# Optimization experiments

Measured on AMD Instinct MI355X. Metric: run time of the kernel, lower is better.

The kernel has to match this reference:

```python
import jax, jax.numpy as jnp
import numpy as np

HIDDEN = 64
N_LAYERS = 3
WORLD_W = 1.0
WORLD_H = 1.0

silu = jax.nn.silu


def _lin(x, w, b):
    return x @ w + b


def setup_inputs() -> dict:
    key = jax.random.key(0)
    ks = jax.random.split(key, 32)
    B, N, H, L = 2, 512, HIDDEN, N_LAYERS
    s = 0.05
    inp = {
        "state": jax.random.uniform(ks[0], (B, N, 4), dtype=jnp.float32),
        "h_init_w": jax.random.normal(ks[1], (1, H), dtype=jnp.float32) * s,
        "h_init_b": jnp.zeros((H,), jnp.float32),
        # per-layer stacked params (L, ...)
        "edge_w1": jax.random.normal(ks[2], (L, 2 * H + 4, H), jnp.float32) * s,
        "edge_b1": jnp.zeros((L, H), jnp.float32),
        "edge_w2": jax.random.normal(ks[3], (L, H, H), jnp.float32) * s,
        "edge_b2": jnp.zeros((L, H), jnp.float32),
        "force_w1": jax.random.normal(ks[4], (L, H, H), jnp.float32) * s,
        "force_b1": jnp.zeros((L, H), jnp.float32),
        "force_w2": jax.random.normal(ks[5], (L, H, 1), jnp.float32) * s,
        "force_b2": jnp.zeros((L, 1), jnp.float32),
        "node_w1": jax.random.normal(ks[6], (L, 2 * H, H), jnp.float32) * s,
        "node_b1": jnp.zeros((L, H), jnp.float32),
        "node_w2": jax.random.normal(ks[7], (L, H, H), jnp.float32) * s,
        "node_b2": jnp.zeros((L, H), jnp.float32),
        "wall_w1": jax.random.normal(ks[8], (H + 4, H), jnp.float32) * s,
        "wall_b1": jnp.zeros((H,), jnp.float32),
        "wall_w2": jax.random.normal(ks[9], (H, H), jnp.float32) * s,
        "wall_b2": jnp.zeros((H,), jnp.float32),
        "wall_w3": jax.random.normal(ks[10], (H, 4), jnp.float32) * s,
        "wall_b3": jnp.zeros((4,), jnp.float32),
    }
    return inp


def _layer(h, pos, vel, ew1, eb1, ew2, eb2, fw1, fb1, fw2, fb2, nw1, nb1, nw2, nb2):
    B, N, H = h.shape
    # rel_pos[b,i,j] = pos[b,j] - pos[b,i]
    rel_pos = pos[:, None, :, :] - pos[:, :, None, :]          # (B,N,N,2)
    dist_sq = jnp.sum(rel_pos ** 2, axis=-1, keepdims=True)    # (B,N,N,1)
    dist = jnp.sqrt(dist_sq + 1e-8)
    normal = rel_pos / dist
    speed_sq = jnp.sum(vel ** 2, axis=-1, keepdims=True)       # (B,N,1)
    rel_vel = vel[:, None, :, :] - vel[:, :, None, :]
    approach = jnp.sum(rel_vel * normal, axis=-1, keepdims=True)
    h_i = jnp.broadcast_to(h[:, :, None, :], (B, N, N, H))
    h_j = jnp.broadcast_to(h[:, None, :, :], (B, N, N, H))
    sp_i = jnp.broadcast_to(speed_sq[:, :, None, :], (B, N, N, 1))
    sp_j = jnp.broadcast_to(speed_sq[:, None, :, :], (B, N, N, 1))
    edge_feat = jnp.concatenate([h_i, h_j, dist_sq, sp_i, sp_j, approach], axis=-1)
    m_ij = silu(_lin(silu(_lin(edge_feat, ew1, eb1)), ew2, eb2))  # (B,N,N,H)
    force_weight = _lin(silu(_lin(m_ij, fw1, fb1)), fw2, fb2)     # (B,N,N,1)
    mask = (1.0 - jnp.eye(N, dtype=h.dtype))[None, :, :, None]
    force = jnp.sum(force_weight * normal * mask, axis=2)         # (B,N,2)
    m_agg = jnp.sum(m_ij * mask, axis=2)                          # (B,N,H)
    h_new = _lin(silu(_lin(jnp.concatenate([h, m_agg], axis=-1), nw1, nb1)), nw2, nb2)
    return h_new, force


def reference(state, h_init_w, h_init_b, edge_w1, edge_b1, edge_w2, edge_b2,
              force_w1, force_b1, force_w2, force_b2,
              node_w1, node_b1, node_w2, node_b2,
              wall_w1, wall_b1, wall_w2, wall_b2, wall_w3, wall_b3):
    pos = state[:, :, :2]
    vel = state[:, :, 2:]
    speed = jnp.sqrt(jnp.sum(vel ** 2, axis=-1, keepdims=True))
    h = silu(_lin(speed, h_init_w, h_init_b))
    total_force = jnp.zeros_like(pos)
    for l in range(edge_w1.shape[0]):
        h, f = _layer(h, pos, vel,
                      edge_w1[l], edge_b1[l], edge_w2[l], edge_b2[l],
                      force_w1[l], force_b1[l], force_w2[l], force_b2[l],
                      node_w1[l], node_b1[l], node_w2[l], node_b2[l])
        total_force = total_force + f
    wall_dists = jnp.stack([pos[:, :, 0], WORLD_W - pos[:, :, 0],
                            pos[:, :, 1], WORLD_H - pos[:, :, 1]], axis=-1)
    x = jnp.concatenate([h, wall_dists], axis=-1)
    wall_mag = _lin(silu(_lin(silu(_lin(x, wall_w1, wall_b1)), wall_w2, wall_b2)), wall_w3, wall_b3)  # (B,N,4)
    wall_normals = jnp.array([[1.0, 0.0], [-1.0, 0.0], [0.0, 1.0], [0.0, -1.0]], dtype=state.dtype)
    wall_force = jnp.einsum('bnw,wd->bnd', wall_mag, wall_normals)
    return total_force + wall_force
```

## Files before the change

### kernel.cpp

```cpp
#include <hip/hip_runtime.h>
#include <math.h>

#define H 64
#define NN 512
#define NB 2
#define NL 3
#define NBLK (NN * NB)

typedef _Float16 half8  __attribute__((ext_vector_type(8)));
typedef __fp16   fp16x2 __attribute__((ext_vector_type(2)));
typedef float    float4v __attribute__((ext_vector_type(4)));

union FragU { half8 h; unsigned int u[4]; uint4 q4; };
union F8    { float4 v4[2]; float f[8]; };

__device__ __forceinline__ float silu_f(float x) {
    float e = __expf(-x);
    return x * __builtin_amdgcn_rcpf(1.0f + e);
}

__device__ __forceinline__ unsigned int pk2(float a, float b) {
    fp16x2 h = __builtin_amdgcn_cvt_pkrtz(a, b);
    return __builtin_bit_cast(unsigned int, h);
}

__global__ __launch_bounds__(256) void k_setup(
    const float* __restrict__ state, const float* __restrict__ hiw,
    const float* __restrict__ hib, const float* __restrict__ ew1,
    const float* __restrict__ eb1, const float* __restrict__ ew2,
    const float* __restrict__ fw1, float* __restrict__ h,
    float* __restrict__ P, float* __restrict__ Q, float* __restrict__ faccum,
    uint4* __restrict__ wpack)
{
    const int bn  = blockIdx.x;
    const int tid = threadIdx.x;
    const int wv  = tid >> 6;
    const int lane = tid & 63;

    __shared__ float sh[64];
    __shared__ float sRed[4][64];
    __shared__ float sRedQ[4][64];

    if (tid < 64) {
        const float* st = state + bn * 4;
        float vx = st[2], vy = st[3];
        float s2 = vx * vx + vy * vy;
        if (tid < 2) faccum[bn * 2 + tid] = 0.0f;
        float hv = silu_f(sqrtf(s2) * hiw[tid] + hib[tid]);
        h[(size_t)bn * H + tid] = hv;
        sh[tid] = hv;
    }
    if (bn < 6) {
        const int pl = bn >> 1, mat = bn & 1;
        const float* src = (mat ? fw1 : ew2) + (size_t)pl * 4096;
        uint4* dst = wpack + ((size_t)pl * 2 + mat) * 512;
        for (int g = tid; g < 512; g += 256) {
            int f = g >> 6, ln = g & 63;
            int mt = f >> 1, kt = f & 1, qq = ln >> 4, mm = ln & 15;
            int cm  = mt * 16 + mm;
            int cin = kt * 32 + qq * 8;
            uint4 u;
            u.x = pk2(src[(cin + 0) * 64 + cm], src[(cin + 1) * 64 + cm]);
            u.y = pk2(src[(cin + 2) * 64 + cm], src[(cin + 3) * 64 + cm]);
            u.z = pk2(src[(cin + 4) * 64 + cm], src[(cin + 5) * 64 + cm]);
            u.w = pk2(src[(cin + 6) * 64 + cm], src[(cin + 7) * 64 + cm]);
            dst[g] = u;
        }
    }
    __syncthreads();

    {
        float pp = 0.0f, qp = 0.0f;
        const float* wp = ew1 + (size_t)(wv * 16) * 64 + lane;
        const float* wq = ew1 + (size_t)(64 + wv * 16) * 64 + lane;
#pragma unroll 8
        for (int k = 0; k < 16; k++) {
            float hk = sh[wv * 16 + k];
            pp += hk * wp[(size_t)k * 64];
            qp += hk * wq[(size_t)k * 64];
        }
        sRed[wv][lane]  = pp;
        sRedQ[wv][lane] = qp;
    }
    __syncthreads();
    if (wv == 0) {
        const float* st = state + bn * 4;
        float vx = st[2], vy = st[3];
        float s2 = vx * vx + vy * vy;
        P[(size_t)bn * 64 + lane] = eb1[lane] + sRed[0][lane] + sRed[1][lane]
                                  + sRed[2][lane] + sRed[3][lane];
        Q[(size_t)bn * 64 + lane] = sRedQ[0][lane] + sRedQ[1][lane]
                                  + sRedQ[2][lane] + sRedQ[3][lane]
                                  + s2 * ew1[130 * 64 + lane];
    }
}

__global__ __launch_bounds__(256) void k_edge(
    const float* __restrict__ state,
    const float* __restrict__ P, const float* __restrict__ Q,
    float* __restrict__ Pout, float* __restrict__ Qout,
    const float* __restrict__ ew1_l,
    const uint4* __restrict__ wpackL,
    const float* __restrict__ eb2_l,
    const float* __restrict__ fb1_l,
    const float* __restrict__ fw2_l, const float* __restrict__ fb2_l,
    float* __restrict__ h, float* __restrict__ faccum,
    const float* __restrict__ nw1_l, const float* __restrict__ nb1_l,
    const float* __restrict__ nw2_l, const float* __restrict__ nb2_l,
    const float* __restrict__ ew1_n, const float* __restrict__ eb1_n,
    const float* __restrict__ ww1, const float* __restrict__ wb1,
    const float* __restrict__ ww2, const float* __restrict__ wb2,
    const float* __restrict__ ww3, const float* __restrict__ wb3,
    float* __restrict__ out, int last)
{
    const int i    = blockIdx.x;
    const int b    = blockIdx.y;
    const int tid  = threadIdx.x;
    const int wv   = tid >> 6;
    const int lane = tid & 63;
    const int q    = lane >> 4;
    const int m    = lane & 15;
    const int bn_i = b * NN + i;

    __shared__ float sW[128];
    __shared__ float sBias[192];
    __shared__ float sPB[64];
    __shared__ unsigned short sMT[4][16 * 72];
    __shared__ float sRed[4][64];
    __shared__ float sRedQ[4][64];
    __shared__ float sF[4][2];

    if (tid < 128) sW[tid] = ew1_l[(128 + (tid >> 6) * 3) * 64 + (tid & 63)];
    if (tid < 192) sBias[tid] = (tid < 64) ? eb2_l[tid]
                              : (tid < 128) ? fb1_l[tid - 64]
                              : fw2_l[tid - 128];

    FragU wreg[8], freg[8];
#pragma unroll
    for (int f = 0; f < 8; f++) {
        wreg[f].q4 = wpackL[f * 64 + lane];
        freg[f].q4 = wpackL[512 + f * 64 + lane];
    }

    const float4 sti = *(const float4*)&state[(size_t)bn_i * 4];
    const float  spi = sti.z * sti.z + sti.w * sti.w;
    if (tid < 64) sPB[tid] = P[(size_t)bn_i * 64 + tid] + spi * ew1_l[129 * 64 + tid];
    __syncthreads();

    const float fb2q = fb2_l[0] * 0.25f;

    float maccp[16];
#pragma unroll
    for (int t = 0; t < 16; t++) maccp[t] = 0.0f;
    float fax = 0.0f, fay = 0.0f;

    unsigned short* MT = sMT[wv];

#pragma unroll 1
    for (int ck = 0; ck < 8; ck++) {
        unsigned swoff = 0;
        asm volatile("" : "+v"(swoff));
        __builtin_assume((swoff & 3u) == 0);

        const int jg = wv * 128 + ck * 16 + m;

        float jnx, jny;
        FragU xb[2];
        {
            const float4 stj = *(const float4*)&state[(size_t)(b * NN + jg) * 4];
            float dx = stj.x - sti.x, dy = stj.y - sti.y;
            float ds = dx * dx + dy * dy;
            float rs = __builtin_amdgcn_rsqf(ds + 1e-8f);
            jnx = dx * rs;
            jny = dy * rs;
            float jap = (stj.z - sti.z) * jnx + (stj.w - sti.w) * jny;

#pragma unroll
            for (int kt = 0; kt < 2; kt++) {
                const int c0 = kt * 32 + q * 8;
                F8 w0, w3, pb;
                w0.v4[0] = *(const float4*)&sW[swoff + c0];
                w0.v4[1] = *(const float4*)&sW[swoff + c0 + 4];
                w3.v4[0] = *(const float4*)&sW[swoff + 64 + c0];
                w3.v4[1] = *(const float4*)&sW[swoff + 64 + c0 + 4];
                pb.v4[0] = *(const float4*)&sPB[swoff + c0];
                pb.v4[1] = *(const float4*)&sPB[swoff + c0 + 4];

                const float* Qr = &Q[(size_t)(b * NN + jg) * 64 + c0];
                F8 qv;
                qv.v4[0] = *(const float4*)Qr;
                qv.v4[1] = *(const float4*)(Qr + 4);
                float xv[8];
#pragma unroll
                for (int d = 0; d < 8; d++) {
                    float pre = pb.f[d] + qv.f[d] + ds * w0.f[d]
                              + jap * w3.f[d];
                    xv[d] = silu_f(pre);
                }
#pragma unroll
                for (int d = 0; d < 4; d++)
                    xb[kt].u[d] = pk2(xv[2 * d], xv[2 * d + 1]);
            }
        }

#pragma unroll
        for (int hf = 0; hf < 2; hf++) {
            float4v acc[2];
#pragma unroll
            for (int mt2 = 0; mt2 < 2; mt2++) {
                const float4 b2v = *(const float4*)&sBias[swoff + (hf * 2 + mt2) * 16 + q * 4];
                acc[mt2][0] = b2v.x; acc[mt2][1] = b2v.y;
                acc[mt2][2] = b2v.z; acc[mt2][3] = b2v.w;
            }
#pragma unroll
            for (int kt = 0; kt < 2; kt++) {
#pragma unroll
                for (int mt2 = 0; mt2 < 2; mt2++) {
                    acc[mt2] = __builtin_amdgcn_mfma_f32_16x16x32_f16(
                        wreg[(hf * 2 + mt2) * 2 + kt].h, xb[kt].h, acc[mt2], 0, 0, 0);
                }
            }
#pragma unroll
            for (int mt2 = 0; mt2 < 2; mt2++) {
                const int mt = hf * 2 + mt2;
                float4v a = acc[mt2];
                float m0 = silu_f(a[0]);
                float m1 = silu_f(a[1]);
                float m2 = silu_f(a[2]);
                float m3 = silu_f(a[3]);
                if (jg != i) {
                    maccp[mt * 4 + 0] += m0;
                    maccp[mt * 4 + 1] += m1;
                    maccp[mt * 4 + 2] += m2;
                    maccp[mt * 4 + 3] += m3;
                }
                uint2 dw = make_uint2(pk2(m0, m1), pk2(m2, m3));
                *(uint2*)&MT[m * 72 + mt * 16 + q * 4] = dw;
            }
        }

        float fdp = 0.0f;
        FragU xb2[2];
#pragma unroll
        for (int kt = 0; kt < 2; kt++)
            xb2[kt].q4 = *(uint4*)&MT[m * 72 + kt * 32 + q * 8];
#pragma unroll
        for (int hf = 0; hf < 2; hf++) {
            float4v acc2[2];
#pragma unroll
            for (int mt2 = 0; mt2 < 2; mt2++) {
                const float4 fb1v = *(const float4*)&sBias[swoff + 64 + (hf * 2 + mt2) * 16 + q * 4];
                acc2[mt2][0] = fb1v.x; acc2[mt2][1] = fb1v.y;
                acc2[mt2][2] = fb1v.z; acc2[mt2][3] = fb1v.w;
            }
#pragma unroll
            for (int kt = 0; kt < 2; kt++) {
#pragma unroll
                for (int mt2 = 0; mt2 < 2; mt2++) {
                    acc2[mt2] = __builtin_amdgcn_mfma_f32_16x16x32_f16(
                        freg[(hf * 2 + mt2) * 2 + kt].h, xb2[kt].h, acc2[mt2], 0, 0, 0);
                }
            }
#pragma unroll
            for (int mt2 = 0; mt2 < 2; mt2++) {
                const float4 fw2v = *(const float4*)&sBias[swoff + 128 + (hf * 2 + mt2) * 16 + q * 4];
                float4v a = acc2[mt2];
                fdp += silu_f(a[0]) * fw2v.x
                     + silu_f(a[1]) * fw2v.y
                     + silu_f(a[2]) * fw2v.z
                     + silu_f(a[3]) * fw2v.w;
            }
        }

        {
            float fd = fdp + fb2q;
            fax += fd * jnx;
            fay += fd * jny;
        }
    }

#pragma unroll
    for (int t = 0; t < 16; t++) {
        float v = maccp[t];
        v += __shfl_xor(v, 1, 64);
        v += __shfl_xor(v, 2, 64);
        v += __shfl_xor(v, 4, 64);
        v += __shfl_xor(v, 8, 64);
        maccp[t] = v;
    }
    if (m == 0) {
#pragma unroll
        for (int mt = 0; mt < 4; mt++)
#pragma unroll
          for (int r = 0; r < 4; r++)
            sRed[wv][mt * 16 + q * 4 + r] = maccp[mt * 4 + r];
    }
#pragma unroll
    for (int off = 1; off < 64; off <<= 1) {
        fax += __shfl_xor(fax, off, 64);
        fay += __shfl_xor(fay, off, 64);
    }
    if (lane == 0) {
        sF[wv][0] = fax;
        sF[wv][1] = fay;
    }
    __syncthreads();

    float* scr = (float*)sMT;
    const int c = lane;
    if (wv == 0) {
        float magg = sRed[0][c] + sRed[1][c] + sRed[2][c] + sRed[3][c];
        scr[c]      = h[(size_t)bn_i * 64 + c];
        scr[64 + c] = magg;
    }
    __syncthreads();

    {
        float part = 0.0f;
        const float* w = nw1_l + (size_t)(wv * 32) * 64 + c;
#pragma unroll 8
        for (int k = 0; k < 32; k++) part += scr[wv * 32 + k] * w[(size_t)k * 64];
        sRed[wv][c] = part;
    }
    __syncthreads();
    if (wv == 0) {
        float t1 = nb1_l[c] + sRed[0][c] + sRed[1][c] + sRed[2][c] + sRed[3][c];
        scr[128 + c] = silu_f(t1);
    }
    __syncthreads();

    {
        float part = 0.0f;
        const float* w = nw2_l + (size_t)(wv * 16) * 64 + c;
#pragma unroll 8
        for (int k = 0; k < 16; k++) part += scr[128 + wv * 16 + k] * w[(size_t)k * 64];
        sRed[wv][c] = part;
    }
    __syncthreads();

    if (wv == 0) {
        float hn  = nb2_l[c] + sRed[0][c] + sRed[1][c] + sRed[2][c] + sRed[3][c];
        scr[192 + c] = hn;
        if (!last) {
            h[(size_t)bn_i * 64 + c] = hn;
            float fxl = sF[0][0] + sF[1][0] + sF[2][0] + sF[3][0];
            float fyl = sF[0][1] + sF[1][1] + sF[2][1] + sF[3][1];
            if (c == 0) {
                faccum[bn_i * 2 + 0] += fxl;
                faccum[bn_i * 2 + 1] += fyl;
            }
        }
    }
    __syncthreads();

    if (!last) {
        float pp = 0.0f, qp = 0.0f;
        const float* wp = ew1_n + (size_t)(wv * 16) * 64 + c;
        const float* wq = ew1_n + (size_t)(64 + wv * 16) * 64 + c;
#pragma unroll 8
        for (int k = 0; k < 16; k++) {
            float hk = scr[192 + wv * 16 + k];
            pp += hk * wp[(size_t)k * 64];
            qp += hk * wq[(size_t)k * 64];
        }
        sRed[wv][c]  = pp;
        sRedQ[wv][c] = qp;
        __syncthreads();
        if (wv == 0) {
            Pout[(size_t)bn_i * 64 + c] = eb1_n[c] + sRed[0][c] + sRed[1][c]
                                        + sRed[2][c] + sRed[3][c];
            Qout[(size_t)bn_i * 64 + c] = sRedQ[0][c] + sRedQ[1][c]
                                        + sRedQ[2][c] + sRedQ[3][c]
                                        + spi * ew1_n[130 * 64 + c];
        }
        return;
    }

    if (wv != 0) return;

    if (c < 4) {
        float px = sti.x, py = sti.y;
        float wd = (c == 0) ? px : (c == 1) ? 1.0f - px : (c == 2) ? py : 1.0f - py;
        scr[256 + c] = wd;
    }
    float t2 = wb1[c];
#pragma unroll 4
    for (int k = 0; k < 64; k++) t2 += scr[192 + k] * ww1[k * 64 + c];
#pragma unroll
    for (int k = 0; k < 4; k++)  t2 += scr[256 + k] * ww1[(64 + k) * 64 + c];
    t2 = silu_f(t2);
    scr[320 + c] = t2;
    float u = wb2[c];
#pragma unroll 8
    for (int k = 0; k < 64; k++) u += scr[320 + k] * ww2[k * 64 + c];
    u = silu_f(u);
    scr[384 + c] = u;
    if (c < 4) {
        float mg = wb3[c];
        for (int k = 0; k < 64; k++) mg += scr[384 + k] * ww3[k * 4 + c];
        scr[448 + c] = mg;
    }
    if (c == 0) {
        float fxl = sF[0][0] + sF[1][0] + sF[2][0] + sF[3][0];
        float fyl = sF[0][1] + sF[1][1] + sF[2][1] + sF[3][1];
        float fx = faccum[bn_i * 2 + 0] + fxl + (scr[448 + 0] - scr[448 + 1]);
        float fy = faccum[bn_i * 2 + 1] + fyl + (scr[448 + 2] - scr[448 + 3]);
        out[bn_i * 2 + 0] = fx;
        out[bn_i * 2 + 1] = fy;
    }
}

extern "C" void kernel_launch(void* const* d_in, const int* in_sizes, int n_in,
                              void* d_out, int out_size, void* d_ws, size_t ws_size,
                              hipStream_t stream)
{
    const float* state = (const float*)d_in[0];
    const float* hiw   = (const float*)d_in[1];
    const float* hib   = (const float*)d_in[2];
    const float* ew1   = (const float*)d_in[3];
    const float* eb1   = (const float*)d_in[4];
    const float* ew2   = (const float*)d_in[5];
    const float* eb2   = (const float*)d_in[6];
    const float* fw1   = (const float*)d_in[7];
    const float* fb1   = (const float*)d_in[8];
    const float* fw2   = (const float*)d_in[9];
    const float* fb2   = (const float*)d_in[10];
    const float* nw1   = (const float*)d_in[11];
    const float* nb1   = (const float*)d_in[12];
    const float* nw2   = (const float*)d_in[13];
    const float* nb2   = (const float*)d_in[14];
    const float* ww1   = (const float*)d_in[15];
    const float* wb1   = (const float*)d_in[16];
    const float* ww2   = (const float*)d_in[17];
    const float* wb2   = (const float*)d_in[18];
    const float* ww3   = (const float*)d_in[19];
    const float* wb3   = (const float*)d_in[20];
    float* out = (float*)d_out;

    float* ws     = (float*)d_ws;
    float* h      = ws;
    float* P0     = h      + (size_t)NB * NN * H;
    float* Q0     = P0     + (size_t)NB * NN * H;
    float* P1     = Q0     + (size_t)NB * NN * H;
    float* Q1     = P1     + (size_t)NB * NN * H;
    float* faccum = Q1     + (size_t)NB * NN * H;
    float* wpackf = faccum + (size_t)NB * NN * 2;
    uint4* wpack  = (uint4*)(((uintptr_t)wpackf + 15) & ~(uintptr_t)15);

    float* Pb[2] = { P0, P1 };
    float* Qb[2] = { Q0, Q1 };

    k_setup<<<NBLK, 256, 0, stream>>>(state, hiw, hib, ew1, eb1,
                                      ew2, fw1, h, P0, Q0, faccum, wpack);

    for (int l = 0; l < NL; l++) {
        const int last = (l == NL - 1) ? 1 : 0;
        const int nl = last ? 0 : (l + 1);
        const int cur = l & 1, nxt = (l + 1) & 1;
        k_edge<<<dim3(NN, NB), 256, 0, stream>>>(
            state, Pb[cur], Qb[cur], Pb[nxt], Qb[nxt],
            ew1 + (size_t)l * 132 * 64,
            wpack + (size_t)l * 1024,
            eb2 + (size_t)l * 64,
            fb1 + (size_t)l * 64,
            fw2 + (size_t)l * 64, fb2 + (size_t)l,
            h, faccum,
            nw1 + (size_t)l * 128 * 64, nb1 + (size_t)l * 64,
            nw2 + (size_t)l * 64 * 64,  nb2 + (size_t)l * 64,
            ew1 + (size_t)nl * 132 * 64, eb1 + (size_t)nl * 64,
            ww1, wb1, ww2, wb2, ww3, wb3,
            out, last);
    }
}
```

Measured before the change: 236.8 us.

## Software-pipeline edge MLP chunks with double-buffered LDS tile

Restructures the per-wave chunk loop into a front stage (edge features plus first MFMA layer, writing to LDS) and a back stage (force MLP reading the previous chunk's tile). LDS is double-buffered so the force stage of chunk ck-1 can interleave with the edge stage of chunk ck, hiding the LDS write-to-read latency and the MFMA dependency chains. It also adds a min-blocks-per-CU hint of 4 to launch_bounds. In exchange the kernel uses more LDS and carries fragments across iterations, which raises register pressure and could cause spills under the tighter occupancy bound.

```diff
diff --git a/kernel.cpp b/kernel.cpp
--- a/kernel.cpp
+++ b/kernel.cpp
@@ -95,7 +95,7 @@
     }
 }
 
-__global__ __launch_bounds__(256) void k_edge(
+__global__ __launch_bounds__(256, 4) void k_edge(
     const float* __restrict__ state,
     const float* __restrict__ P, const float* __restrict__ Q,
     float* __restrict__ Pout, float* __restrict__ Qout,
@@ -125,7 +125,7 @@
     __shared__ float sW[128];
     __shared__ float sBias[192];
     __shared__ float sPB[64];
-    __shared__ unsigned short sMT[4][16 * 72];
+    __shared__ __align__(16) unsigned short sMTd[2][4][16 * 72];
     __shared__ float sRed[4][64];
     __shared__ float sRedQ[4][64];
     __shared__ float sF[4][2];
@@ -154,26 +154,25 @@
     for (int t = 0; t < 16; t++) maccp[t] = 0.0f;
     float fax = 0.0f, fay = 0.0f;
 
-    unsigned short* MT = sMT[wv];
-
-#pragma unroll 1
-    for (int ck = 0; ck < 8; ck++) {
+    FragU xb2[2];
+    float pjnx, pjny;
+
+    auto do_front = [&](int ck, float& jnx_o, float& jny_o) {
         unsigned swoff = 0;
         asm volatile("" : "+v"(swoff));
         __builtin_assume((swoff & 3u) == 0);
 
         const int jg = wv * 128 + ck * 16 + m;
 
-        float jnx, jny;
         FragU xb[2];
         {
             const float4 stj = *(const float4*)&state[(size_t)(b * NN + jg) * 4];
             float dx = stj.x - sti.x, dy = stj.y - sti.y;
             float ds = dx * dx + dy * dy;
             float rs = __builtin_amdgcn_rsqf(ds + 1e-8f);
-            jnx = dx * rs;
-            jny = dy * rs;
-            float jap = (stj.z - sti.z) * jnx + (stj.w - sti.w) * jny;
+            jnx_o = dx * rs;
+            jny_o = dy * rs;
+            float jap = (stj.z - sti.z) * jnx_o + (stj.w - sti.w) * jny_o;
 
 #pragma unroll
             for (int kt = 0; kt < 2; kt++) {
@@ -202,6 +201,8 @@
                     xb[kt].u[d] = pk2(xv[2 * d], xv[2 * d + 1]);
             }
         }
+
+        unsigned short* MT = sMTd[ck & 1][wv];
 
 #pragma unroll
         for (int hf = 0; hf < 2; hf++) {
@@ -238,12 +239,14 @@
                 *(uint2*)&MT[m * 72 + mt * 16 + q * 4] = dw;
             }
         }
+    };
+
+    auto do_back = [&](float jnxp, float jnyp) {
+        unsigned swoff = 0;
+        asm volatile("" : "+v"(swoff));
+        __builtin_assume((swoff & 3u) == 0);
 
         float fdp = 0.0f;
-        FragU xb2[2];
-#pragma unroll
-        for (int kt = 0; kt < 2; kt++)
-            xb2[kt].q4 = *(uint4*)&MT[m * 72 + kt * 32 + q * 8];
 #pragma unroll
         for (int hf = 0; hf < 2; hf++) {
             float4v acc2[2];
@@ -271,12 +274,29 @@
                      + silu_f(a[3]) * fw2v.w;
             }
         }
-
+        float fd = fdp + fb2q;
+        fax += fd * jnxp;
+        fay += fd * jnyp;
+    };
+
+    do_front(0, pjnx, pjny);
+#pragma unroll 1
+    for (int ck = 1; ck < 8; ck++) {
         {
-            float fd = fdp + fb2q;
-            fax += fd * jnx;
-            fay += fd * jny;
-        }
+            const unsigned short* MTp = sMTd[(ck + 1) & 1][wv];
+            xb2[0].q4 = *(const uint4*)&MTp[m * 72 + q * 8];
+            xb2[1].q4 = *(const uint4*)&MTp[m * 72 + 32 + q * 8];
+        }
+        float jnx, jny;
+        do_front(ck, jnx, jny);
+        do_back(pjnx, pjny);
+        pjnx = jnx; pjny = jny;
+    }
+    {
+        const unsigned short* MTp = sMTd[1][wv];
+        xb2[0].q4 = *(const uint4*)&MTp[m * 72 + q * 8];
+        xb2[1].q4 = *(const uint4*)&MTp[m * 72 + 32 + q * 8];
+        do_back(pjnx, pjny);
     }
 
 #pragma unroll
@@ -306,7 +326,7 @@
     }
     __syncthreads();
 
-    float* scr = (float*)sMT;
+    float* scr = (float*)sMTd;
     const int c = lane;
     if (wv == 0) {
         float magg = sRed[0][c] + sRed[1][c] + sRed[2][c] + sRed[3][c];
```

After: 289.0 us. 22.0% more time.

## Process two receiver nodes per block with 512 threads to share neighbor loads

Applied to the files above, without the earlier changes.

Each k_edge block now handles two i-nodes with eight waves instead of one node with four waves. Every wave sweeps 64 neighbors and reuses each neighbor's state and Q row for both nodes. The node-update tail is split so that each group of four waves serves one node. The aim is to halve per-block setup work (weight fragment loads, bias staging) and the global Q traffic per pair. In exchange, registers and LDS per block roughly double, which may lower occupancy, and the grid shrinks to 512 blocks.

```diff
diff --git a/kernel.cpp b/kernel.cpp
--- a/kernel.cpp
+++ b/kernel.cpp
@@ -95,7 +95,7 @@
     }
 }
 
-__global__ __launch_bounds__(256) void k_edge(
+__global__ __launch_bounds__(512) void k_edge(
     const float* __restrict__ state,
     const float* __restrict__ P, const float* __restrict__ Q,
     float* __restrict__ Pout, float* __restrict__ Qout,
@@ -113,22 +113,22 @@
     const float* __restrict__ ww3, const float* __restrict__ wb3,
     float* __restrict__ out, int last)
 {
-    const int i    = blockIdx.x;
+    const int ip   = blockIdx.x;
     const int b    = blockIdx.y;
     const int tid  = threadIdx.x;
     const int wv   = tid >> 6;
     const int lane = tid & 63;
     const int q    = lane >> 4;
     const int m    = lane & 15;
-    const int bn_i = b * NN + i;
+    const int bn0  = b * NN + ip * 2;
 
     __shared__ float sW[128];
     __shared__ float sBias[192];
-    __shared__ float sPB[64];
-    __shared__ unsigned short sMT[4][16 * 72];
-    __shared__ float sRed[4][64];
-    __shared__ float sRedQ[4][64];
-    __shared__ float sF[4][2];
+    __shared__ float sPB[2][64];
+    __shared__ __align__(16) unsigned short sMT[8][2][16 * 72];
+    __shared__ float sRed[2][8][64];
+    __shared__ float sRedQ[2][4][64];
+    __shared__ float sF[8][4];
 
     if (tid < 128) sW[tid] = ew1_l[(128 + (tid >> 6) * 3) * 64 + (tid & 63)];
     if (tid < 192) sBias[tid] = (tid < 64) ? eb2_l[tid]
@@ -142,212 +142,255 @@
         freg[f].q4 = wpackL[512 + f * 64 + lane];
     }
 
-    const float4 sti = *(const float4*)&state[(size_t)bn_i * 4];
-    const float  spi = sti.z * sti.z + sti.w * sti.w;
-    if (tid < 64) sPB[tid] = P[(size_t)bn_i * 64 + tid] + spi * ew1_l[129 * 64 + tid];
+    const float4 sti0 = *(const float4*)&state[(size_t)bn0 * 4];
+    const float4 sti1 = *(const float4*)&state[(size_t)(bn0 + 1) * 4];
+    const float  spi0 = sti0.z * sti0.z + sti0.w * sti0.w;
+    const float  spi1 = sti1.z * sti1.z + sti1.w * sti1.w;
+    if (tid < 128) {
+        const int ci = tid >> 6, c = tid & 63;
+        const float sp = ci ? spi1 : spi0;
+        sPB[ci][c] = P[(size_t)(bn0 + ci) * 64 + c] + sp * ew1_l[129 * 64 + c];
+    }
     __syncthreads();
 
     const float fb2q = fb2_l[0] * 0.25f;
 
-    float maccp[16];
-#pragma unroll
-    for (int t = 0; t < 16; t++) maccp[t] = 0.0f;
-    float fax = 0.0f, fay = 0.0f;
-
-    unsigned short* MT = sMT[wv];
+    float maccp[2][16];
+#pragma unroll
+    for (int ii = 0; ii < 2; ii++)
+#pragma unroll
+        for (int t = 0; t < 16; t++) maccp[ii][t] = 0.0f;
+    float fax[2] = {0.0f, 0.0f}, fay[2] = {0.0f, 0.0f};
 
 #pragma unroll 1
-    for (int ck = 0; ck < 8; ck++) {
+    for (int ck = 0; ck < 4; ck++) {
         unsigned swoff = 0;
         asm volatile("" : "+v"(swoff));
         __builtin_assume((swoff & 3u) == 0);
 
-        const int jg = wv * 128 + ck * 16 + m;
-
-        float jnx, jny;
-        FragU xb[2];
+        const int jg = wv * 64 + ck * 16 + m;
+
+        const float4 stj = *(const float4*)&state[(size_t)(b * NN + jg) * 4];
+        float jnx[2], jny[2], dsv[2], jap[2];
         {
-            const float4 stj = *(const float4*)&state[(size_t)(b * NN + jg) * 4];
-            float dx = stj.x - sti.x, dy = stj.y - sti.y;
-            float ds = dx * dx + dy * dy;
-            float rs = __builtin_amdgcn_rsqf(ds + 1e-8f);
-            jnx = dx * rs;
-            jny = dy * rs;
-            float jap = (stj.z - sti.z) * jnx + (stj.w - sti.w) * jny;
-
-#pragma unroll
-            for (int kt = 0; kt < 2; kt++) {
-                const int c0 = kt * 32 + q * 8;
-                F8 w0, w3, pb;
-                w0.v4[0] = *(const float4*)&sW[swoff + c0];
-                w0.v4[1] = *(const float4*)&sW[swoff + c0 + 4];
-                w3.v4[0] = *(const float4*)&sW[swoff + 64 + c0];
-                w3.v4[1] = *(const float4*)&sW[swoff + 64 + c0 + 4];
-                pb.v4[0] = *(const float4*)&sPB[swoff + c0];
-                pb.v4[1] = *(const float4*)&sPB[swoff + c0 + 4];
-
-                const float* Qr = &Q[(size_t)(b * NN + jg) * 64 + c0];
-                F8 qv;
-                qv.v4[0] = *(const float4*)Qr;
-                qv.v4[1] = *(const float4*)(Qr + 4);
-                float xv[8];
-#pragma unroll
-                for (int d = 0; d < 8; d++) {
-                    float pre = pb.f[d] + qv.f[d] + ds * w0.f[d]
-                              + jap * w3.f[d];
-                    xv[d] = silu_f(pre);
-                }
-#pragma unroll
-                for (int d = 0; d < 4; d++)
-                    xb[kt].u[d] = pk2(xv[2 * d], xv[2 * d + 1]);
+            float dx = stj.x - sti0.x, dy = stj.y - sti0.y;
+            float d2 = dx * dx + dy * dy;
+            float rs = __builtin_amdgcn_rsqf(d2 + 1e-8f);
+            jnx[0] = dx * rs; jny[0] = dy * rs; dsv[0] = d2;
+            jap[0] = (stj.z - sti0.z) * jnx[0] + (stj.w - sti0.w) * jny[0];
+        }
+        {
+            float dx = stj.x - sti1.x, dy = stj.y - sti1.y;
+            float d2 = dx * dx + dy * dy;
+            float rs = __builtin_amdgcn_rsqf(d2 + 1e-8f);
+            jnx[1] = dx * rs; jny[1] = dy * rs; dsv[1] = d2;
+            jap[1] = (stj.z - sti1.z) * jnx[1] + (stj.w - sti1.w) * jny[1];
+        }
+
+        FragU xb[2][2];
+#pragma unroll
+        for (int kt = 0; kt < 2; kt++) {
+            const int c0 = kt * 32 + q * 8;
+            F8 w0, w3, pb0, pb1;
+            w0.v4[0] = *(const float4*)&sW[swoff + c0];
+            w0.v4[1] = *(const float4*)&sW[swoff + c0 + 4];
+            w3.v4[0] = *(const float4*)&sW[swoff + 64 + c0];
+            w3.v4[1] = *(const float4*)&sW[swoff + 64 + c0 + 4];
+            pb0.v4[0] = *(const float4*)&sPB[0][swoff + c0];
+            pb0.v4[1] = *(const float4*)&sPB[0][swoff + c0 + 4];
+            pb1.v4[0] = *(const float4*)&sPB[1][swoff + c0];
+            pb1.v4[1] = *(const float4*)&sPB[1][swoff + c0 + 4];
+
+            const float* Qr = &Q[(size_t)(b * NN + jg) * 64 + c0];
+            F8 qv;
+            qv.v4[0] = *(const float4*)Qr;
+            qv.v4[1] = *(const float4*)(Qr + 4);
+
+            float xv0[8], xv1[8];
+#pragma unroll
+            for (int d = 0; d < 8; d++) {
+                float base = qv.f[d];
+                float w0d = w0.f[d], w3d = w3.f[d];
+                float pre0 = pb0.f[d] + base + dsv[0] * w0d + jap[0] * w3d;
+                float pre1 = pb1.f[d] + base + dsv[1] * w0d + jap[1] * w3d;
+                xv0[d] = silu_f(pre0);
+                xv1[d] = silu_f(pre1);
             }
-        }
-
-#pragma unroll
-        for (int hf = 0; hf < 2; hf++) {
-            float4v acc[2];
-#pragma unroll
-            for (int mt2 = 0; mt2 < 2; mt2++) {
-                const float4 b2v = *(const float4*)&sBias[swoff + (hf * 2 + mt2) * 16 + q * 4];
-                acc[mt2][0] = b2v.x; acc[mt2][1] = b2v.y;
-                acc[mt2][2] = b2v.z; acc[mt2][3] = b2v.w;
+#pragma unroll
+            for (int d = 0; d < 4; d++) {
+                xb[0][kt].u[d] = pk2(xv0[2 * d], xv0[2 * d + 1]);
+                xb[1][kt].u[d] = pk2(xv1[2 * d], xv1[2 * d + 1]);
             }
-#pragma unroll
-            for (int kt = 0; kt < 2; kt++) {
+        }
+
+#pragma unroll
+        for (int ii = 0; ii < 2; ii++) {
+            unsigned short* MT = sMT[wv][ii];
+            const int inode = ip * 2 + ii;
+#pragma unroll
+            for (int hf = 0; hf < 2; hf++) {
+                float4v acc[2];
 #pragma unroll
                 for (int mt2 = 0; mt2 < 2; mt2++) {
-                    acc[mt2] = __builtin_amdgcn_mfma_f32_16x16x32_f16(
-                        wreg[(hf * 2 + mt2) * 2 + kt].h, xb[kt].h, acc[mt2], 0, 0, 0);
+                    const float4 b2v = *(const float4*)&sBias[swoff + (hf * 2 + mt2) * 16 + q * 4];
+                    acc[mt2][0] = b2v.x; acc[mt2][1] = b2v.y;
+                    acc[mt2][2] = b2v.z; acc[mt2][3] = b2v.w;
+                }
+#pragma unroll
+                for (int kt = 0; kt < 2; kt++) {
+#pragma unroll
+                    for (int mt2 = 0; mt2 < 2; mt2++) {
+                        acc[mt2] = __builtin_amdgcn_mfma_f32_16x16x32_f16(
+                            wreg[(hf * 2 + mt2) * 2 + kt].h, xb[ii][kt].h, acc[mt2], 0, 0, 0);
+                    }
+                }
+#pragma unroll
+                for (int mt2 = 0; mt2 < 2; mt2++) {
+                    const int mt = hf * 2 + mt2;
+                    float4v a = acc[mt2];
+                    float m0 = silu_f(a[0]);
+                    float m1 = silu_f(a[1]);
+                    float m2 = silu_f(a[2]);
+                    float m3 = silu_f(a[3]);
+                    if (jg != inode) {
+                        maccp[ii][mt * 4 + 0] += m0;
+                        maccp[ii][mt * 4 + 1] += m1;
+                        maccp[ii][mt * 4 + 2] += m2;
+                        maccp[ii][mt * 4 + 3] += m3;
+                    }
+                    uint2 dw = make_uint2(pk2(m0, m1), pk2(m2, m3));
+                    *(uint2*)&MT[m * 72 + mt * 16 + q * 4] = dw;
                 }
             }
-#pragma unroll
-            for (int mt2 = 0; mt2 < 2; mt2++) {
-                const int mt = hf * 2 + mt2;
-                float4v a = acc[mt2];
-                float m0 = silu_f(a[0]);
-                float m1 = silu_f(a[1]);
-                float m2 = silu_f(a[2]);
-                float m3 = silu_f(a[3]);
-                if (jg != i) {
-                    maccp[mt * 4 + 0] += m0;
-                    maccp[mt * 4 + 1] += m1;
-                    maccp[mt * 4 + 2] += m2;
-                    maccp[mt * 4 + 3] += m3;
-                }
-                uint2 dw = make_uint2(pk2(m0, m1), pk2(m2, m3));
-                *(uint2*)&MT[m * 72 + mt * 16 + q * 4] = dw;
+        }
+
+#pragma unroll
+        for (int ii = 0; ii < 2; ii++) {
+            const unsigned short* MT = sMT[wv][ii];
+            FragU xb2[2];
+            xb2[0].q4 = *(const uint4*)&MT[m * 72 + q * 8];
+            xb2[1].q4 = *(const uint4*)&MT[m * 72 + 32 + q * 8];
+            float fdp = 0.0f;
+#pragma unroll
+            for (int hf = 0; hf < 2; hf++) {
+                float4v acc2[2];
+#pragma unroll
+                for (int mt2 = 0; mt2 < 2; mt2++) {
+                    const float4 fb1v = *(const float4*)&sBias[swoff + 64 + (hf * 2 + mt2) * 16 + q * 4];
+                    acc2[mt2][0] = fb1v.x; acc2[mt2][1] = fb1v.y;
+                    acc2[mt2][2] = fb1v.z; acc2[mt2][3] = fb1v.w;
+                }
+#pragma unroll
+                for (int kt = 0; kt < 2; kt++) {
+#pragma unroll
+                    for (int mt2 = 0; mt2 < 2; mt2++) {
+                        acc2[mt2] = __builtin_amdgcn_mfma_f32_16x16x32_f16(
+                            freg[(hf * 2 + mt2) * 2 + kt].h, xb2[kt].h, acc2[mt2], 0, 0, 0);
+                    }
+                }
+#pragma unroll
+                for (int mt2 = 0; mt2 < 2; mt2++) {
+                    const float4 fw2v = *(const float4*)&sBias[swoff + 128 + (hf * 2 + mt2) * 16 + q * 4];
+                    float4v a = acc2[mt2];
+                    fdp += silu_f(a[0]) * fw2v.x
+                         + silu_f(a[1]) * fw2v.y
+                         + silu_f(a[2]) * fw2v.z
+                         + silu_f(a[3]) * fw2v.w;
+                }
             }
-        }
-
-        float fdp = 0.0f;
-        FragU xb2[2];
-#pragma unroll
-        for (int kt = 0; kt < 2; kt++)
-            xb2[kt].q4 = *(uint4*)&MT[m * 72 + kt * 32 + q * 8];
-#pragma unroll
-        for (int hf = 0; hf < 2; hf++) {
-            float4v acc2[2];
-#pragma unroll
-            for (int mt2 = 0; mt2 < 2; mt2++) {
-                const float4 fb1v = *(const float4*)&sBias[swoff + 64 + (hf * 2 + mt2) * 16 + q * 4];
-                acc2[mt2][0] = fb1v.x; acc2[mt2][1] = fb1v.y;
-                acc2[mt2][2] = fb1v.z; acc2[mt2][3] = fb1v.w;
-            }
-#pragma unroll
-            for (int kt = 0; kt < 2; kt++) {
-#pragma unroll
-                for (int mt2 = 0; mt2 < 2; mt2++) {
-                    acc2[mt2] = __builtin_amdgcn_mfma_f32_16x16x32_f16(
-                        freg[(hf * 2 + mt2) * 2 + kt].h, xb2[kt].h, acc2[mt2], 0, 0, 0);
-                }
-            }
-#pragma unroll
-            for (int mt2 = 0; mt2 < 2; mt2++) {
-                const float4 fw2v = *(const float4*)&sBias[swoff + 128 + (hf * 2 + mt2) * 16 + q * 4];
-                float4v a = acc2[mt2];
-                fdp += silu_f(a[0]) * fw2v.x
-                     + silu_f(a[1]) * fw2v.y
-                     + silu_f(a[2]) * fw2v.z
-                     + silu_f(a[3]) * fw2v.w;
-            }
-        }
-
-        {
             float fd = fdp + fb2q;
-            fax += fd * jnx;
-            fay += fd * jny;
-        }
-    }
-
-#pragma unroll
-    for (int t = 0; t < 16; t++) {
-        float v = maccp[t];
-        v += __shfl_xor(v, 1, 64);
-        v += __shfl_xor(v, 2, 64);
-        v += __shfl_xor(v, 4, 64);
-        v += __shfl_xor(v, 8, 64);
-        maccp[t] = v;
-    }
+            fax[ii] += fd * jnx[ii];
+            fay[ii] += fd * jny[ii];
+        }
+    }
+
+#pragma unroll
+    for (int ii = 0; ii < 2; ii++)
+#pragma unroll
+        for (int t = 0; t < 16; t++) {
+            float v = maccp[ii][t];
+            v += __shfl_xor(v, 1, 64);
+            v += __shfl_xor(v, 2, 64);
+            v += __shfl_xor(v, 4, 64);
+            v += __shfl_xor(v, 8, 64);
+            maccp[ii][t] = v;
+        }
     if (m == 0) {
 #pragma unroll
-        for (int mt = 0; mt < 4; mt++)
-#pragma unroll
-          for (int r = 0; r < 4; r++)
-            sRed[wv][mt * 16 + q * 4 + r] = maccp[mt * 4 + r];
+        for (int ii = 0; ii < 2; ii++)
+#pragma unroll
+            for (int mt = 0; mt < 4; mt++)
+#pragma unroll
+                for (int r = 0; r < 4; r++)
+                    sRed[ii][wv][mt * 16 + q * 4 + r] = maccp[ii][mt * 4 + r];
     }
 #pragma unroll
     for (int off = 1; off < 64; off <<= 1) {
-        fax += __shfl_xor(fax, off, 64);
-        fay += __shfl_xor(fay, off, 64);
+        fax[0] += __shfl_xor(fax[0], off, 64);
+        fay[0] += __shfl_xor(fay[0], off, 64);
+        fax[1] += __shfl_xor(fax[1], off, 64);
+        fay[1] += __shfl_xor(fay[1], off, 64);
     }
     if (lane == 0) {
-        sF[wv][0] = fax;
-        sF[wv][1] = fay;
-    }
-    __syncthreads();
-
-    float* scr = (float*)sMT;
+        sF[wv][0] = fax[0]; sF[wv][1] = fay[0];
+        sF[wv][2] = fax[1]; sF[wv][3] = fay[1];
+    }
+    __syncthreads();
+
+    const int ii  = wv >> 2;
+    const int wv4 = wv & 3;
+    const int bnI = bn0 + ii;
+    float* scrI = ((float*)sMT) + ii * 1024;
     const int c = lane;
-    if (wv == 0) {
-        float magg = sRed[0][c] + sRed[1][c] + sRed[2][c] + sRed[3][c];
-        scr[c]      = h[(size_t)bn_i * 64 + c];
-        scr[64 + c] = magg;
+
+    if (wv4 == 0) {
+        float magg = 0.0f;
+#pragma unroll
+        for (int w = 0; w < 8; w++) magg += sRed[ii][w][c];
+        scrI[c]      = h[(size_t)bnI * 64 + c];
+        scrI[64 + c] = magg;
     }
     __syncthreads();
 
     {
         float part = 0.0f;
-        const float* w = nw1_l + (size_t)(wv * 32) * 64 + c;
+        const float* w = nw1_l + (size_t)(wv4 * 32) * 64 + c;
 #pragma unroll 8
-        for (int k = 0; k < 32; k++) part += scr[wv * 32 + k] * w[(size_t)k * 64];
-        sRed[wv][c] = part;
-    }
-    __syncthreads();
-    if (wv == 0) {
-        float t1 = nb1_l[c] + sRed[0][c] + sRed[1][c] + sRed[2][c] + sRed[3][c];
-        scr[128 + c] = silu_f(t1);
+        for (int k = 0; k < 32; k++) part += scrI[wv4 * 32 + k] * w[(size_t)k * 64];
+        sRed[ii][wv4][c] = part;
+    }
+    __syncthreads();
+    if (wv4 == 0) {
+        float t1 = nb1_l[c] + sRed[ii][0][c] + sRed[ii][1][c]
+                 + sRed[ii][2][c] + sRed[ii][3][c];
+        scrI[128 + c] = silu_f(t1);
     }
     __syncthreads();
 
     {
         float part = 0.0f;
-        const float* w = nw2_l + (size_t)(wv * 16) * 64 + c;
+        const float* w = nw2_l + (size_t)(wv4 * 16) * 64 + c;
 #pragma unroll 8
-        for (int k = 0; k < 16; k++) part += scr[128 + wv * 16 + k] * w[(size_t)k * 64];
-        sRed[wv][c] = part;
-    }
-    __syncthreads();
-
-    if (wv == 0) {
-        float hn  = nb2_l[c] + sRed[0][c] + sRed[1][c] + sRed[2][c] + sRed[3][c];
-        scr[192 + c] = hn;
+        for (int k = 0; k < 16; k++) part += scrI[128 + wv4 * 16 + k] * w[(size_t)k * 64];
+        sRed[ii][wv4][c] = part;
+    }
+    __syncthreads();
+
+    if (wv4 == 0) {
+        float hn = nb2_l[c] + sRed[ii][0][c] + sRed[ii][1][c]
+                 + sRed[ii][2][c] + sRed[ii][3][c];
+        scrI[192 + c] = hn;
         if (!last) {
-            h[(size_t)bn_i * 64 + c] = hn;
-            float fxl = sF[0][0] + sF[1][0] + sF[2][0] + sF[3][0];
-            float fyl = sF[0][1] + sF[1][1] + sF[2][1] + sF[3][1];
+            h[(size_t)bnI * 64 + c] = hn;
             if (c == 0) {
-                faccum[bn_i * 2 + 0] += fxl;
-                faccum[bn_i * 2 + 1] += fyl;
+                float fxl = 0.0f, fyl = 0.0f;
+#pragma unroll
+                for (int w = 0; w < 8; w++) {
+                    fxl += sF[w][ii * 2 + 0];
+                    fyl += sF[w][ii * 2 + 1];
+                }
+                faccum[bnI * 2 + 0] += fxl;
+                faccum[bnI * 2 + 1] += fyl;
             }
         }
     }
@@ -355,58 +398,67 @@
 
     if (!last) {
         float pp = 0.0f, qp = 0.0f;
-        const float* wp = ew1_n + (size_t)(wv * 16) * 64 + c;
-        const float* wq = ew1_n + (size_t)(64 + wv * 16) * 64 + c;
+        const float* wp = ew1_n + (size_t)(wv4 * 16) * 64 + c;
+        const float* wq = ew1_n + (size_t)(64 + wv4 * 16) * 64 + c;
 #pragma unroll 8
         for (int k = 0; k < 16; k++) {
-            float hk = scr[192 + wv * 16 + k];
+            float hk = scrI[192 + wv4 * 16 + k];
             pp += hk * wp[(size_t)k * 64];
             qp += hk * wq[(size_t)k * 64];
         }
-        sRed[wv][c]  = pp;
-        sRedQ[wv][c] = qp;
+        sRed[ii][wv4][c]  = pp;
+        sRedQ[ii][wv4][c] = qp;
         __syncthreads();
-        if (wv == 0) {
-            Pout[(size_t)bn_i * 64 + c] = eb1_n[c] + sRed[0][c] + sRed[1][c]
-                                        + sRed[2][c] + sRed[3][c];
-            Qout[(size_t)bn_i * 64 + c] = sRedQ[0][c] + sRedQ[1][c]
-                                        + sRedQ[2][c] + sRedQ[3][c]
-                                        + spi * ew1_n[130 * 64 + c];
+        if (wv4 == 0) {
+            const float spiI = ii ? spi1 : spi0;
+            Pout[(size_t)bnI * 64 + c] = eb1_n[c] + sRed[ii][0][c] + sRed[ii][1][c]
+                                       + sRed[ii][2][c] + sRed[ii][3][c];
+            Qout[(size_t)bnI * 64 + c] = sRedQ[ii][0][c] + sRedQ[ii][1][c]
+                                       + sRedQ[ii][2][c] + sRedQ[ii][3][c]
+                                       + spiI * ew1_n[130 * 64 + c];
         }
         return;
     }
 
-    if (wv != 0) return;
-
-    if (c < 4) {
-        float px = sti.x, py = sti.y;
-        float wd = (c == 0) ? px : (c == 1) ? 1.0f - px : (c == 2) ? py : 1.0f - py;
-        scr[256 + c] = wd;
+    if (wv4 != 0) return;
+
+    {
+        const float pxI = ii ? sti1.x : sti0.x;
+        const float pyI = ii ? sti1.y : sti0.y;
+        if (c < 4) {
+            float wd = (c == 0) ? pxI : (c == 1) ? 1.0f - pxI
+                     : (c == 2) ? pyI : 1.0f - pyI;
+            scrI[256 + c] = wd;
+        }
     }
     float t2 = wb1[c];
 #pragma unroll 4
-    for (int k = 0; k < 64; k++) t2 += scr[192 + k] * ww1[k * 64 + c];
-#pragma unroll
-    for (int k = 0; k < 4; k++)  t2 += scr[256 + k] * ww1[(64 + k) * 64 + c];
+    for (int k = 0; k < 64; k++) t2 += scrI[192 + k] * ww1[k * 64 + c];
+#pragma unroll
+    for (int k = 0; k < 4; k++)  t2 += scrI[256 + k] * ww1[(64 + k) * 64 + c];
     t2 = silu_f(t2);
-    scr[320 + c] = t2;
+    scrI[320 + c] = t2;
     float u = wb2[c];
 #pragma unroll 8
-    for (int k = 0; k < 64; k++) u += scr[320 + k] * ww2[k * 64 + c];
+    for (int k = 0; k < 64; k++) u += scrI[320 + k] * ww2[k * 64 + c];
     u = silu_f(u);
-    scr[384 + c] = u;
+    scrI[384 + c] = u;
     if (c < 4) {
         float mg = wb3[c];
-        for (int k = 0; k < 64; k++) mg += scr[384 + k] * ww3[k * 4 + c];
-        scr[448 + c] = mg;
+        for (int k = 0; k < 64; k++) mg += scrI[384 + k] * ww3[k * 4 + c];
+        scrI[448 + c] = mg;
     }
     if (c == 0) {
-        float fxl = sF[0][0] + sF[1][0] + sF[2][0] + sF[3][0];
-        float fyl = sF[0][1] + sF[1][1] + sF[2][1] + sF[3][1];
-        float fx = faccum[bn_i * 2 + 0] + fxl + (scr[448 + 0] - scr[448 + 1]);
-        float fy = faccum[bn_i * 2 + 1] + fyl + (scr[448 + 2] - scr[448 + 3]);
-        out[bn_i * 2 + 0] = fx;
-        out[bn_i * 2 + 1] = fy;
+        float fxl = 0.0f, fyl = 0.0f;
+#pragma unroll
+        for (int w = 0; w < 8; w++) {
+            fxl += sF[w][ii * 2 + 0];
+            fyl += sF[w][ii * 2 + 1];
+        }
+        float fx = faccum[bnI * 2 + 0] + fxl + (scrI[448 + 0] - scrI[448 + 1]);
+        float fy = faccum[bnI * 2 + 1] + fyl + (scrI[448 + 2] - scrI[448 + 3]);
+        out[bnI * 2 + 0] = fx;
+        out[bnI * 2 + 1] = fy;
     }
 }
 
@@ -457,7 +509,7 @@
         const int last = (l == NL - 1) ? 1 : 0;
         const int nl = last ? 0 : (l + 1);
         const int cur = l & 1, nxt = (l + 1) & 1;
-        k_edge<<<dim3(NN, NB), 256, 0, stream>>>(
+        k_edge<<<dim3(NN / 2, NB), 512, 0, stream>>>(
             state, Pb[cur], Qb[cur], Pb[nxt], Qb[nxt],
             ew1 + (size_t)l * 132 * 64,
             wpack + (size_t)l * 1024,
```

Measured after the change: 243.5 us. 2.8% more time.

## Split each node's edge loop across two blocks with atomic last-block reduction

Applied to the files above, without the earlier changes.

Doubles the edge-kernel grid so each node's 512 neighbours are split between two blocks, each handling 256 j's. Partial message sums and forces are combined through global atomics, and a per-node counter picks the last-finishing block to run the node MLP and produce the next P/Q. The second-stage MFMA weight fragments move from registers into LDS to lower register pressure. The aim is more parallelism and occupancy per layer. The cost is extra global atomics, a threadfence, zero-initialised scratch buffers, and more LDS use.

```diff
diff --git a/kernel.cpp b/kernel.cpp
--- a/kernel.cpp
+++ b/kernel.cpp
@@ -30,7 +30,8 @@
     const float* __restrict__ eb1, const float* __restrict__ ew2,
     const float* __restrict__ fw1, float* __restrict__ h,
     float* __restrict__ P, float* __restrict__ Q, float* __restrict__ faccum,
-    uint4* __restrict__ wpack)
+    uint4* __restrict__ wpack, float* __restrict__ mpart,
+    unsigned* __restrict__ cntb)
 {
     const int bn  = blockIdx.x;
     const int tid = threadIdx.x;
@@ -40,6 +41,9 @@
     __shared__ float sh[64];
     __shared__ float sRed[4][64];
     __shared__ float sRedQ[4][64];
+
+    if (tid < 192) mpart[((size_t)(tid >> 6) * NBLK + bn) * 64 + (tid & 63)] = 0.0f;
+    if (tid >= 192 && tid < 195) cntb[(size_t)(tid - 192) * NBLK + bn] = 0u;
 
     if (tid < 64) {
         const float* st = state + bn * 4;
@@ -105,6 +109,7 @@
     const float* __restrict__ fb1_l,
     const float* __restrict__ fw2_l, const float* __restrict__ fb2_l,
     float* __restrict__ h, float* __restrict__ faccum,
+    float* __restrict__ mpartL, unsigned* __restrict__ cntL,
     const float* __restrict__ nw1_l, const float* __restrict__ nb1_l,
     const float* __restrict__ nw2_l, const float* __restrict__ nb2_l,
     const float* __restrict__ ew1_n, const float* __restrict__ eb1_n,
@@ -114,7 +119,9 @@
     float* __restrict__ out, int last)
 {
     const int i    = blockIdx.x;
-    const int b    = blockIdx.y;
+    const int bh   = blockIdx.y;
+    const int b    = bh >> 1;
+    const int half = bh & 1;
     const int tid  = threadIdx.x;
     const int wv   = tid >> 6;
     const int lane = tid & 63;
@@ -125,22 +132,23 @@
     __shared__ float sW[128];
     __shared__ float sBias[192];
     __shared__ float sPB[64];
-    __shared__ unsigned short sMT[4][16 * 72];
+    __shared__ __align__(16) unsigned short sMT[4][16 * 72];
+    __shared__ uint4 sFreg[512];
     __shared__ float sRed[4][64];
     __shared__ float sRedQ[4][64];
     __shared__ float sF[4][2];
+    __shared__ int   sLast;
 
     if (tid < 128) sW[tid] = ew1_l[(128 + (tid >> 6) * 3) * 64 + (tid & 63)];
     if (tid < 192) sBias[tid] = (tid < 64) ? eb2_l[tid]
                               : (tid < 128) ? fb1_l[tid - 64]
                               : fw2_l[tid - 128];
 
-    FragU wreg[8], freg[8];
-#pragma unroll
-    for (int f = 0; f < 8; f++) {
-        wreg[f].q4 = wpackL[f * 64 + lane];
-        freg[f].q4 = wpackL[512 + f * 64 + lane];
-    }
+    FragU wreg[8];
+#pragma unroll
+    for (int f = 0; f < 8; f++) wreg[f].q4 = wpackL[f * 64 + lane];
+    sFreg[tid]       = wpackL[512 + tid];
+    sFreg[256 + tid] = wpackL[512 + 256 + tid];
 
     const float4 sti = *(const float4*)&state[(size_t)bn_i * 4];
     const float  spi = sti.z * sti.z + sti.w * sti.w;
@@ -154,15 +162,13 @@
     for (int t = 0; t < 16; t++) maccp[t] = 0.0f;
     float fax = 0.0f, fay = 0.0f;
 
-    unsigned short* MT = sMT[wv];
-
 #pragma unroll 1
-    for (int ck = 0; ck < 8; ck++) {
+    for (int ck = 0; ck < 4; ck++) {
         unsigned swoff = 0;
         asm volatile("" : "+v"(swoff));
         __builtin_assume((swoff & 3u) == 0);
 
-        const int jg = wv * 128 + ck * 16 + m;
+        const int jg = half * 256 + wv * 64 + ck * 16 + m;
 
         float jnx, jny;
         FragU xb[2];
@@ -202,6 +208,8 @@
                     xb[kt].u[d] = pk2(xv[2 * d], xv[2 * d + 1]);
             }
         }
+
+        unsigned short* MT = sMT[wv];
 
 #pragma unroll
         for (int hf = 0; hf < 2; hf++) {
@@ -257,8 +265,10 @@
             for (int kt = 0; kt < 2; kt++) {
 #pragma unroll
                 for (int mt2 = 0; mt2 < 2; mt2++) {
+                    FragU fr;
+                    fr.q4 = sFreg[swoff + ((hf * 2 + mt2) * 2 + kt) * 64 + lane];
                     acc2[mt2] = __builtin_amdgcn_mfma_f32_16x16x32_f16(
-                        freg[(hf * 2 + mt2) * 2 + kt].h, xb2[kt].h, acc2[mt2], 0, 0, 0);
+                        fr.h, xb2[kt].h, acc2[mt2], 0, 0, 0);
                 }
             }
 #pragma unroll
@@ -306,12 +316,29 @@
     }
     __syncthreads();
 
-    float* scr = (float*)sMT;
     const int c = lane;
     if (wv == 0) {
         float magg = sRed[0][c] + sRed[1][c] + sRed[2][c] + sRed[3][c];
+        atomicAdd(&mpartL[(size_t)bn_i * 64 + c], magg);
+        if (lane == 0) {
+            float fxl = sF[0][0] + sF[1][0] + sF[2][0] + sF[3][0];
+            float fyl = sF[0][1] + sF[1][1] + sF[2][1] + sF[3][1];
+            atomicAdd(&faccum[bn_i * 2 + 0], fxl);
+            atomicAdd(&faccum[bn_i * 2 + 1], fyl);
+        }
+        __threadfence();
+        if (lane == 0) {
+            unsigned old = atomicAdd(&cntL[bn_i], 1u);
+            sLast = (old == 1) ? 1 : 0;
+        }
+    }
+    __syncthreads();
+    if (!sLast) return;
+
+    float* scr = (float*)sMT;
+    if (wv == 0) {
         scr[c]      = h[(size_t)bn_i * 64 + c];
-        scr[64 + c] = magg;
+        scr[64 + c] = atomicAdd(&mpartL[(size_t)bn_i * 64 + c], 0.0f);
     }
     __syncthreads();
 
@@ -341,15 +368,7 @@
     if (wv == 0) {
         float hn  = nb2_l[c] + sRed[0][c] + sRed[1][c] + sRed[2][c] + sRed[3][c];
         scr[192 + c] = hn;
-        if (!last) {
-            h[(size_t)bn_i * 64 + c] = hn;
-            float fxl = sF[0][0] + sF[1][0] + sF[2][0] + sF[3][0];
-            float fyl = sF[0][1] + sF[1][1] + sF[2][1] + sF[3][1];
-            if (c == 0) {
-                faccum[bn_i * 2 + 0] += fxl;
-                faccum[bn_i * 2 + 1] += fyl;
-            }
-        }
+        if (!last) h[(size_t)bn_i * 64 + c] = hn;
     }
     __syncthreads();
 
@@ -401,12 +420,10 @@
         scr[448 + c] = mg;
     }
     if (c == 0) {
-        float fxl = sF[0][0] + sF[1][0] + sF[2][0] + sF[3][0];
-        float fyl = sF[0][1] + sF[1][1] + sF[2][1] + sF[3][1];
-        float fx = faccum[bn_i * 2 + 0] + fxl + (scr[448 + 0] - scr[448 + 1]);
-        float fy = faccum[bn_i * 2 + 1] + fyl + (scr[448 + 2] - scr[448 + 3]);
-        out[bn_i * 2 + 0] = fx;
-        out[bn_i * 2 + 1] = fy;
+        float fxT = atomicAdd(&faccum[bn_i * 2 + 0], 0.0f);
+        float fyT = atomicAdd(&faccum[bn_i * 2 + 1], 0.0f);
+        out[bn_i * 2 + 0] = fxT + (scr[448 + 0] - scr[448 + 1]);
+        out[bn_i * 2 + 1] = fyT + (scr[448 + 2] - scr[448 + 3]);
     }
 }
 
@@ -446,18 +463,21 @@
     float* faccum = Q1     + (size_t)NB * NN * H;
     float* wpackf = faccum + (size_t)NB * NN * 2;
     uint4* wpack  = (uint4*)(((uintptr_t)wpackf + 15) & ~(uintptr_t)15);
+    float* mpart  = (float*)(wpack + 3 * 1024);
+    unsigned* cntb = (unsigned*)(mpart + (size_t)3 * NBLK * 64);
 
     float* Pb[2] = { P0, P1 };
     float* Qb[2] = { Q0, Q1 };
 
     k_setup<<<NBLK, 256, 0, stream>>>(state, hiw, hib, ew1, eb1,
-                                      ew2, fw1, h, P0, Q0, faccum, wpack);
+                                      ew2, fw1, h, P0, Q0, faccum, wpack,
+                                      mpart, cntb);
 
     for (int l = 0; l < NL; l++) {
         const int last = (l == NL - 1) ? 1 : 0;
         const int nl = last ? 0 : (l + 1);
         const int cur = l & 1, nxt = (l + 1) & 1;
-        k_edge<<<dim3(NN, NB), 256, 0, stream>>>(
+        k_edge<<<dim3(NN, NB * 2), 256, 0, stream>>>(
             state, Pb[cur], Qb[cur], Pb[nxt], Qb[nxt],
             ew1 + (size_t)l * 132 * 64,
             wpack + (size_t)l * 1024,
@@ -465,6 +485,7 @@
             fb1 + (size_t)l * 64,
             fw2 + (size_t)l * 64, fb2 + (size_t)l,
             h, faccum,
+            mpart + (size_t)l * NBLK * 64, cntb + (size_t)l * NBLK,
             nw1 + (size_t)l * 128 * 64, nb1 + (size_t)l * 64,
             nw2 + (size_t)l * 64 * 64,  nb2 + (size_t)l * 64,
             ew1 + (size_t)nl * 132 * 64, eb1 + (size_t)nl * 64,
```

New measurement: 377.0 us. 1.59x slower.
